# Performance work log

Hardware: AMD Instinct MI355X
Metric: run time of the kernel (lower is better)

The kernel has to match this reference:

```python
import jax, jax.numpy as jnp
import numpy as np

FILTER_LEN = 32
SCALE = float(np.sqrt(10 ** (-15 / 10)))  # expected_SI_power_dB = -15


def _fir_valid(x, w):
    """Valid cross-correlation along W axis. x: [B,H,W,1], w: [L] -> [B,H,W-L+1,1].
    Matches Keras Conv2D(kernel_size=(1,L), padding='valid') (cross-correlation)."""
    B, H, W, _ = x.shape
    L = w.shape[0]
    xr = x.reshape(B * H, W, 1)
    k = w.reshape(L, 1, 1)  # (spatial, in, out)
    y = jax.lax.conv_general_dilated(xr, k, window_strides=(1,), padding='VALID',
                                     dimension_numbers=('NWC', 'WIO', 'NWC'))
    return y.reshape(B, H, W - L + 1, 1)


def setup_inputs() -> dict:
    key = jax.random.key(0)
    ks = jax.random.split(key, 10)
    B, H, W = 16, 1, 262144
    f32 = jnp.float32
    return {
        'x_real': jax.random.normal(ks[0], (B, H, W, 1), f32),
        'x_imag': jax.random.normal(ks[1], (B, H, W, 1), f32),
        'w1_pre': jax.random.normal(ks[2], (1, 8), f32) * 0.5,
        'w2_pre': jax.random.normal(ks[3], (8, 1), f32) * 0.5,
        'w_fir_r': jax.random.normal(ks[4], (FILTER_LEN,), f32) * 0.1,
        'w_fir_i': jax.random.normal(ks[5], (FILTER_LEN,), f32) * 0.1,
        'w1_post': jax.random.normal(ks[6], (1, 8), f32) * 0.5,
        'b1_post': jax.random.normal(ks[7], (8,), f32) * 0.1,
        'w2_post': jax.random.normal(ks[8], (8, 1), f32) * 0.5,
        'b2_post': jax.random.normal(ks[9], (1,), f32) * 0.1,
    }


def reference(x_real, x_imag, w1_pre, w2_pre, w_fir_r, w_fir_i,
              w1_post, b1_post, w2_post, b2_post):
    # --- pre nonlinearity on magnitude (1x1 conv MLP: 1 -> 8 tanh -> 1) ---
    x_mag = jnp.sqrt(x_real * x_real + x_imag * x_imag)      # [B,H,W,1]
    x_phase = jnp.arctan2(x_imag, x_real)                    # [B,H,W,1]
    h = jnp.tanh(jnp.einsum('bhwc,cf->bhwf', x_mag, w1_pre))  # [B,H,W,8]
    m = jnp.einsum('bhwf,fc->bhwc', h, w2_pre)               # [B,H,W,1]
    xh_r = m * jnp.cos(x_phase)
    xh_i = m * jnp.sin(x_phase)
    # --- complex FIR (length-32, valid) via 4 real convs ---
    zr = _fir_valid(xh_r, w_fir_r) - _fir_valid(xh_i, w_fir_i)
    zi = _fir_valid(xh_i, w_fir_r) + _fir_valid(xh_r, w_fir_i)
    # --- post nonlinearity on magnitude (1x1 conv MLP: 1 -> 8 relu -> 1) ---
    z_mag = jnp.sqrt(zr * zr + zi * zi)
    z_phase = jnp.arctan2(zi, zr)
    g = jax.nn.relu(jnp.einsum('bhwc,cf->bhwf', z_mag, w1_post) + b1_post)
    zm = jnp.einsum('bhwf,fc->bhwc', g, w2_post) + b2_post
    yr = SCALE * zm * jnp.cos(z_phase)
    yi = SCALE * zm * jnp.sin(z_phase)
    # complex output represented as [real, imag] on last axis: [B,H,W-31,2]
    return jnp.concatenate([yr, yi], axis=-1)
```

## Files before the change

kernel.cpp:

```cpp
#include <hip/hip_runtime.h>

#define TILE   2048
#define NS     2096
#define WIDTH  262144
#define OUTW   (WIDTH - 31)
#define SCALE_V 0.17782794100389229f

#define TBL_N    2048
#define TBL_MAX  10.0f
#define TBL_SCL  (TBL_N / TBL_MAX)

typedef _Float16 half8  __attribute__((ext_vector_type(8)));
typedef _Float16 half4v __attribute__((ext_vector_type(4)));
typedef float    floatx4 __attribute__((ext_vector_type(4)));

__device__ __forceinline__ float wload(const float* __restrict__ w, int t) {
    return (t >= 0 && t < 32) ? w[t] : 0.0f;
}

#define MFMA16(A, B, C) __builtin_amdgcn_mfma_f32_16x16x32_f16((A), (B), (C), 0, 0, 0)

__device__ __forceinline__ float s_of_mag(float mag, const float* w1, const float* w2) {
    if (mag == 0.0f) {
        float s = 0.f;
#pragma unroll
        for (int f = 0; f < 8; ++f) s = fmaf(w2[f], w1[f], s);
        return s;
    }
    float m = 0.f;
#pragma unroll
    for (int f = 0; f < 8; ++f) m = fmaf(w2[f], tanhf(w1[f] * mag), m);
    return m / mag;
}

__global__ void fill_s_table(const float* __restrict__ w1_pre,
                             const float* __restrict__ w2_pre,
                             float2* __restrict__ tbl)
{
    const int i = blockIdx.x * 256 + threadIdx.x;
    if (i >= TBL_N) return;
    float w1[8], w2[8];
#pragma unroll
    for (int f = 0; f < 8; ++f) { w1[f] = w1_pre[f]; w2[f] = w2_pre[f]; }
    const float m0 = (float)i       * (1.0f / TBL_SCL);
    const float m1 = (float)(i + 1) * (1.0f / TBL_SCL);
    const float s0 = s_of_mag(m0, w1, w2);
    const float s1 = s_of_mag(m1, w1, w2);
    tbl[i] = make_float2(s0, s1 - s0);
}

__global__ __launch_bounds__(256) void fused_hammer_mfma(
    const float* __restrict__ xr_g,   const float* __restrict__ xi_g,
    const float* __restrict__ w1_pre, const float* __restrict__ w2_pre,
    const float* __restrict__ wfr,    const float* __restrict__ wfi,
    const float* __restrict__ w1_post,const float* __restrict__ b1_post,
    const float* __restrict__ w2_post,const float* __restrict__ b2_post,
    const float2* __restrict__ tbl_g,
    float* __restrict__ out)
{
    __shared__ __align__(16) _Float16 s_rh[NS];
    __shared__ __align__(16) _Float16 s_rl[NS];
    __shared__ __align__(16) _Float16 s_ih[NS];
    __shared__ __align__(16) _Float16 s_il[NS];
    __shared__ __align__(16) float2   s_tab[TBL_N];

    const int tid    = threadIdx.x;
    const int lane   = tid & 63;
    const int wv     = tid >> 6;
    const int tstart = blockIdx.x * TILE;
    const int brow   = blockIdx.y;
    const long rowbase = (long)brow * WIDTH;

    {
        const float4* src = (const float4*)tbl_g;
#pragma unroll
        for (int q = 0; q < 4; ++q) {
            const int idx = 4 * tid + q;
            ((float4*)s_tab)[idx] = src[idx];
        }
    }

    float w1p[8], b1p[8], w2p[8];
#pragma unroll
    for (int f = 0; f < 8; ++f) { w1p[f] = w1_post[f]; b1p[f] = b1_post[f]; w2p[f] = w2_post[f]; }
    const float b2p = b2_post[0];

    const int jA = lane & 15;
    const int kg = lane >> 4;
    half8 A1r_h, A1r_l, A1mi_h, A1mi_l, A1i_h, A1i_l, A2r_h, A2r_l, A2i_h, A2i_l;
#pragma unroll
    for (int jj = 0; jj < 8; ++jj) {
        const int k  = 8 * kg + jj;
        const int t1 = k - jA;
        const float wr1 = wload(wfr, t1);
        const float wi1 = wload(wfi, t1);
        const int t2 = (k < 16) ? (k + 32 - jA) : (k + 16 - jA);
        const float wr2 = wload(wfr, t2);
        const float wi2 = wload(wfi, t2);
        const float a2r = (k < 16) ? wr2 : -wi2;
        const float a2i = (k < 16) ? wi2 : wr2;
        _Float16 h;
        h = (_Float16)wr1;   A1r_h[jj]  = h; A1r_l[jj]  = (_Float16)(wr1 - (float)h);
        h = (_Float16)(-wi1);A1mi_h[jj] = h; A1mi_l[jj] = (_Float16)(-wi1 - (float)h);
        h = (_Float16)wi1;   A1i_h[jj]  = h; A1i_l[jj]  = (_Float16)(wi1 - (float)h);
        h = (_Float16)a2r;   A2r_h[jj]  = h; A2r_l[jj]  = (_Float16)(a2r - (float)h);
        h = (_Float16)a2i;   A2i_h[jj]  = h; A2i_l[jj]  = (_Float16)(a2i - (float)h);
    }

    __syncthreads();

    for (int p = tid; p < NS / 4; p += 256) {
        const int g = tstart + 4 * p;
        float4 vr, vi;
        if (g + 3 < WIDTH) {
            vr = *(const float4*)(xr_g + rowbase + g);
            vi = *(const float4*)(xi_g + rowbase + g);
        } else {
            float rr[4], ii[4];
#pragma unroll
            for (int e = 0; e < 4; ++e) {
                const int gg = g + e;
                rr[e] = (gg < WIDTH) ? xr_g[rowbase + gg] : 0.f;
                ii[e] = (gg < WIDTH) ? xi_g[rowbase + gg] : 0.f;
            }
            vr = make_float4(rr[0], rr[1], rr[2], rr[3]);
            vi = make_float4(ii[0], ii[1], ii[2], ii[3]);
        }
        const float* vrf = &vr.x;
        const float* vif = &vi.x;
        half4v rh, rl, ih, il;
#pragma unroll
        for (int e = 0; e < 4; ++e) {
            const float r  = vrf[e], im = vif[e];
            const float sq  = fmaf(r, r, im * im);
            const float mag = __builtin_sqrtf(sq);
            const float t   = fminf(mag * TBL_SCL, (float)(TBL_N - 2) + 0.999f);
            const int   i0  = (int)t;
            const float frac = t - (float)i0;
            const float2 en = s_tab[i0];
            const float s   = fmaf(frac, en.y, en.x);
            const float xhr = s * r;
            const float xhi = s * im;
            const _Float16 hr = (_Float16)xhr;
            const _Float16 hi = (_Float16)xhi;
            rh[e] = hr; rl[e] = (_Float16)(xhr - (float)hr);
            ih[e] = hi; il[e] = (_Float16)(xhi - (float)hi);
        }
        *(half4v*)&s_rh[4 * p] = rh;
        *(half4v*)&s_rl[4 * p] = rl;
        *(half4v*)&s_ih[4 * p] = ih;
        *(half4v*)&s_il[4 * p] = il;
    }
    __syncthreads();

#pragma unroll
    for (int tt = 0; tt < 2; ++tt) {
        const int base_o = 512 * wv + 256 * tt;
        const int i1 = base_o + 16 * jA + 8 * kg;
        const half8 Bxr_h = *(const half8*)&s_rh[i1];
        const half8 Bxi_h = *(const half8*)&s_ih[i1];
        const half8 Bxr_l = *(const half8*)&s_rl[i1];
        const half8 Bxi_l = *(const half8*)&s_il[i1];
        const int i2 = base_o + 16 * jA + 32 + 8 * (kg & 1);
        const _Float16* srcH = (kg < 2) ? s_rh : s_ih;
        const _Float16* srcL = (kg < 2) ? s_rl : s_il;
        const half8 Bmx_h = *(const half8*)&srcH[i2];
        const half8 Bmx_l = *(const half8*)&srcL[i2];

        floatx4 accr = {0.f, 0.f, 0.f, 0.f};
        floatx4 acci = {0.f, 0.f, 0.f, 0.f};
        accr = MFMA16(A1r_h,  Bxr_h, accr);  acci = MFMA16(A1i_h,  Bxr_h, acci);
        accr = MFMA16(A1mi_h, Bxi_h, accr);  acci = MFMA16(A1r_h,  Bxi_h, acci);
        accr = MFMA16(A2r_h,  Bmx_h, accr);  acci = MFMA16(A2i_h,  Bmx_h, acci);
        accr = MFMA16(A1r_h,  Bxr_l, accr);  acci = MFMA16(A1i_h,  Bxr_l, acci);
        accr = MFMA16(A1mi_h, Bxi_l, accr);  acci = MFMA16(A1r_h,  Bxi_l, acci);
        accr = MFMA16(A2r_h,  Bmx_l, accr);  acci = MFMA16(A2i_h,  Bmx_l, acci);
        accr = MFMA16(A1r_l,  Bxr_h, accr);  acci = MFMA16(A1i_l,  Bxr_h, acci);
        accr = MFMA16(A1mi_l, Bxi_h, accr);  acci = MFMA16(A1r_l,  Bxi_h, acci);
        accr = MFMA16(A2r_l,  Bmx_h, accr);  acci = MFMA16(A2i_l,  Bmx_h, acci);

        const int obase = tstart + base_o + 16 * jA + 4 * kg;
#pragma unroll
        for (int r = 0; r < 4; ++r) {
            const int o = obase + r;
            if (o < OUTW) {
                const float zr  = accr[r], zi = acci[r];
                const float zsq = fmaf(zr, zr, zi * zi);
                const float rs  = (zsq > 0.f) ? __builtin_amdgcn_rsqf(zsq) : 0.f;
                const float zmag = zsq * rs;
                float zm = b2p;
#pragma unroll
                for (int f = 0; f < 8; ++f) {
                    const float gfv = fmaf(zmag, w1p[f], b1p[f]);
                    zm = fmaf(fmaxf(gfv, 0.f), w2p[f], zm);
                }
                const float t = SCALE_V * zm * rs;
                float2 o2;
                o2.x = (zsq > 0.f) ? t * zr : SCALE_V * zm;
                o2.y = t * zi;
                *(float2*)&out[((long)brow * OUTW + o) * 2] = o2;
            }
        }
    }
}

extern "C" void kernel_launch(void* const* d_in, const int* in_sizes, int n_in,
                              void* d_out, int out_size, void* d_ws, size_t ws_size,
                              hipStream_t stream) {
    float2* tbl = (float2*)d_ws;
    fill_s_table<<<dim3((TBL_N + 255) / 256), 256, 0, stream>>>(
        (const float*)d_in[2], (const float*)d_in[3], tbl);

    const int blocks_w = (OUTW + TILE - 1) / TILE;
    dim3 grid(blocks_w, 16);
    fused_hammer_mfma<<<grid, 256, 0, stream>>>(
        (const float*)d_in[0], (const float*)d_in[1],
        (const float*)d_in[2], (const float*)d_in[3],
        (const float*)d_in[4], (const float*)d_in[5],
        (const float*)d_in[6], (const float*)d_in[7],
        (const float*)d_in[8], (const float*)d_in[9],
        tbl,
        (float*)d_out);
}
```

Before: 112.7 us.

## Give each wave a private input slice, drop block barrier, vectorize output stores

Each of the four waves now loads and preprocesses its own 512-sample slice plus halo into private LDS buffers, so the block-wide barrier after staging becomes a wave-local LDS wait. This lets waves proceed independently, at the cost of recomputing the 48-sample halo per wave. The lookup table is halved to 1024 entries to shrink LDS and its load. Output stores become two float4 writes on even rows, where the alignment allows it.

Measured after the change: 111.5 us. About the same (-1.1%).

```diff
diff --git a/kernel.cpp b/kernel.cpp
--- a/kernel.cpp
+++ b/kernel.cpp
@@ -1,12 +1,13 @@
 #include <hip/hip_runtime.h>
 
 #define TILE   2048
-#define NS     2096
+#define WTILE  512
+#define NSW    560
 #define WIDTH  262144
 #define OUTW   (WIDTH - 31)
 #define SCALE_V 0.17782794100389229f
 
-#define TBL_N    2048
+#define TBL_N    1024
 #define TBL_MAX  10.0f
 #define TBL_SCL  (TBL_N / TBL_MAX)
 
@@ -58,24 +59,25 @@
     const float2* __restrict__ tbl_g,
     float* __restrict__ out)
 {
-    __shared__ __align__(16) _Float16 s_rh[NS];
-    __shared__ __align__(16) _Float16 s_rl[NS];
-    __shared__ __align__(16) _Float16 s_ih[NS];
-    __shared__ __align__(16) _Float16 s_il[NS];
+    __shared__ __align__(16) _Float16 s_rh[4][NSW];
+    __shared__ __align__(16) _Float16 s_rl[4][NSW];
+    __shared__ __align__(16) _Float16 s_ih[4][NSW];
+    __shared__ __align__(16) _Float16 s_il[4][NSW];
     __shared__ __align__(16) float2   s_tab[TBL_N];
 
     const int tid    = threadIdx.x;
     const int lane   = tid & 63;
     const int wv     = tid >> 6;
     const int tstart = blockIdx.x * TILE;
+    const int wstart = tstart + wv * WTILE;
     const int brow   = blockIdx.y;
     const long rowbase = (long)brow * WIDTH;
 
     {
         const float4* src = (const float4*)tbl_g;
 #pragma unroll
-        for (int q = 0; q < 4; ++q) {
-            const int idx = 4 * tid + q;
+        for (int q = 0; q < 2; ++q) {
+            const int idx = 2 * tid + q;
             ((float4*)s_tab)[idx] = src[idx];
         }
     }
@@ -109,8 +111,8 @@
 
     __syncthreads();
 
-    for (int p = tid; p < NS / 4; p += 256) {
-        const int g = tstart + 4 * p;
+    for (int p = lane; p < NSW / 4; p += 64) {
+        const int g = wstart + 4 * p;
         float4 vr, vi;
         if (g + 3 < WIDTH) {
             vr = *(const float4*)(xr_g + rowbase + g);
@@ -146,24 +148,26 @@
             rh[e] = hr; rl[e] = (_Float16)(xhr - (float)hr);
             ih[e] = hi; il[e] = (_Float16)(xhi - (float)hi);
         }
-        *(half4v*)&s_rh[4 * p] = rh;
-        *(half4v*)&s_rl[4 * p] = rl;
-        *(half4v*)&s_ih[4 * p] = ih;
-        *(half4v*)&s_il[4 * p] = il;
-    }
-    __syncthreads();
+        *(half4v*)&s_rh[wv][4 * p] = rh;
+        *(half4v*)&s_rl[wv][4 * p] = rl;
+        *(half4v*)&s_ih[wv][4 * p] = ih;
+        *(half4v*)&s_il[wv][4 * p] = il;
+    }
+    asm volatile("s_waitcnt lgkmcnt(0)" ::: "memory");
+
+    const bool row_aligned = ((brow & 1) == 0);
 
 #pragma unroll
     for (int tt = 0; tt < 2; ++tt) {
-        const int base_o = 512 * wv + 256 * tt;
+        const int base_o = 256 * tt;
         const int i1 = base_o + 16 * jA + 8 * kg;
-        const half8 Bxr_h = *(const half8*)&s_rh[i1];
-        const half8 Bxi_h = *(const half8*)&s_ih[i1];
-        const half8 Bxr_l = *(const half8*)&s_rl[i1];
-        const half8 Bxi_l = *(const half8*)&s_il[i1];
+        const half8 Bxr_h = *(const half8*)&s_rh[wv][i1];
+        const half8 Bxi_h = *(const half8*)&s_ih[wv][i1];
+        const half8 Bxr_l = *(const half8*)&s_rl[wv][i1];
+        const half8 Bxi_l = *(const half8*)&s_il[wv][i1];
         const int i2 = base_o + 16 * jA + 32 + 8 * (kg & 1);
-        const _Float16* srcH = (kg < 2) ? s_rh : s_ih;
-        const _Float16* srcL = (kg < 2) ? s_rl : s_il;
+        const _Float16* srcH = (kg < 2) ? s_rh[wv] : s_ih[wv];
+        const _Float16* srcL = (kg < 2) ? s_rl[wv] : s_il[wv];
         const half8 Bmx_h = *(const half8*)&srcH[i2];
         const half8 Bmx_l = *(const half8*)&srcL[i2];
 
@@ -179,27 +183,39 @@
         accr = MFMA16(A1mi_l, Bxi_h, accr);  acci = MFMA16(A1r_l,  Bxi_h, acci);
         accr = MFMA16(A2r_l,  Bmx_h, accr);  acci = MFMA16(A2i_l,  Bmx_h, acci);
 
-        const int obase = tstart + base_o + 16 * jA + 4 * kg;
+        const int obase = wstart + base_o + 16 * jA + 4 * kg;
+        float ox[8];
 #pragma unroll
         for (int r = 0; r < 4; ++r) {
-            const int o = obase + r;
-            if (o < OUTW) {
-                const float zr  = accr[r], zi = acci[r];
-                const float zsq = fmaf(zr, zr, zi * zi);
-                const float rs  = (zsq > 0.f) ? __builtin_amdgcn_rsqf(zsq) : 0.f;
-                const float zmag = zsq * rs;
-                float zm = b2p;
-#pragma unroll
-                for (int f = 0; f < 8; ++f) {
-                    const float gfv = fmaf(zmag, w1p[f], b1p[f]);
-                    zm = fmaf(fmaxf(gfv, 0.f), w2p[f], zm);
-                }
-                const float t = SCALE_V * zm * rs;
-                float2 o2;
-                o2.x = (zsq > 0.f) ? t * zr : SCALE_V * zm;
-                o2.y = t * zi;
-                *(float2*)&out[((long)brow * OUTW + o) * 2] = o2;
+            const float zr  = accr[r], zi = acci[r];
+            const float zsq = fmaf(zr, zr, zi * zi);
+            const float rs  = (zsq > 0.f) ? __builtin_amdgcn_rsqf(zsq) : 0.f;
+            const float zmag = zsq * rs;
+            float zm = b2p;
+#pragma unroll
+            for (int f = 0; f < 8; ++f) {
+                const float gfv = fmaf(zmag, w1p[f], b1p[f]);
+                zm = fmaf(fmaxf(gfv, 0.f), w2p[f], zm);
             }
+            const float t = SCALE_V * zm * rs;
+            ox[2 * r]     = (zsq > 0.f) ? t * zr : SCALE_V * zm;
+            ox[2 * r + 1] = t * zi;
+        }
+        float* po = &out[((long)brow * OUTW + obase) * 2];
+        if (obase + 3 < OUTW) {
+            if (row_aligned) {
+                *(float4*)(po)     = make_float4(ox[0], ox[1], ox[2], ox[3]);
+                *(float4*)(po + 4) = make_float4(ox[4], ox[5], ox[6], ox[7]);
+            } else {
+#pragma unroll
+                for (int r = 0; r < 4; ++r)
+                    *(float2*)(po + 2 * r) = make_float2(ox[2 * r], ox[2 * r + 1]);
+            }
+        } else {
+#pragma unroll
+            for (int r = 0; r < 4; ++r)
+                if (obase + r < OUTW)
+                    *(float2*)(po + 2 * r) = make_float2(ox[2 * r], ox[2 * r + 1]);
         }
     }
 }
```
